# Performance work log

Hardware: AMD Instinct MI355X
Metric: run time of the kernel (lower is better)

The kernel has to match this reference:

```python
import jax, jax.numpy as jnp
import numpy as np

T, B, DIN, DLAT = 512, 128, 256, 512

def setup_inputs() -> dict:
    key = jax.random.key(0)
    k1, k2, k3, k4, k5 = jax.random.split(key, 5)
    s_i = 1.0 / np.sqrt(DIN)
    s_h = 1.0 / np.sqrt(DLAT)
    return {
        "X": jax.random.normal(k1, (T, B, DIN), dtype=jnp.float32),
        "h": jnp.zeros((B, DLAT), dtype=jnp.float32),
        "Wi": jax.random.uniform(k2, (DLAT, DIN), jnp.float32, -s_i, s_i),
        "bi": jax.random.uniform(k3, (DLAT,), jnp.float32, -s_i, s_i),
        "Wh": jax.random.uniform(k4, (DLAT, DLAT), jnp.float32, -s_h, s_h),
        "bh": jax.random.uniform(k5, (DLAT,), jnp.float32, -s_h, s_h),
    }

def reference(X, h, Wi, bi, Wh, bh):
    # Precompute input projection for all timesteps at once: [T,B,DLAT]
    Xi = jnp.einsum('tbd,ld->tbl', X, Wi) + bi + bh
    def step(h_prev, xi_t):
        h_t = jnp.tanh(xi_t + h_prev @ Wh.T)  # [B, DLAT]
        return h_t, h_t
    _, H = jax.lax.scan(step, h, Xi)
    return H  # [T, B, DLAT]
```

## Files before the change

kernel.cpp:

```cpp
#include <hip/hip_runtime.h>

#define T_STEPS 512
#define BATCH   128
#define DIN     256
#define DLAT    512

typedef __bf16 bf16x8 __attribute__((ext_vector_type(8)));
typedef float  f32x4  __attribute__((ext_vector_type(4)));
typedef int    i32x4  __attribute__((ext_vector_type(4)));
typedef unsigned long long u64;

__device__ __forceinline__ unsigned int f2bf2(float a, float b) {
  unsigned int ua = __float_as_uint(a);
  unsigned int ub = __float_as_uint(b);
  ua = (ua + 0x7FFFu + ((ua >> 16) & 1u)) >> 16;
  ub = (ub + 0x7FFFu + ((ub >> 16) & 1u)) >> 16;
  return ua | (ub << 16);
}

__device__ __forceinline__ uint4 pack8(float4 f0, float4 f1) {
  uint4 r;
  r.x = f2bf2(f0.x, f0.y);
  r.y = f2bf2(f0.z, f0.w);
  r.z = f2bf2(f1.x, f1.y);
  r.w = f2bf2(f1.z, f1.w);
  return r;
}

extern "C" __global__ __launch_bounds__(256) void pk_wh(
    const float* __restrict__ Wh, unsigned int* __restrict__ out) {
  int idx = blockIdx.x * 256 + threadIdx.x;
  const float* src = Wh + (long)idx * 8;
  float4 f0 = *(const float4*)src;
  float4 f1 = *(const float4*)(src + 4);
  uint4 v = pack8(f0, f1);
  *(uint4*)(out + (long)idx * 4) = v;
}

extern "C" __global__ __launch_bounds__(256) void xi_gemm(
    const float* __restrict__ X, const float* __restrict__ Wi,
    const float* __restrict__ bi, const float* __restrict__ bh,
    float* __restrict__ XiOut) {
  extern __shared__ char smem[];
  char*  sX    = smem;
  char*  sW    = smem + 65536;
  float* sBias = (float*)(smem + 131072);

  const int tid = threadIdx.x;
  const long m0 = (long)blockIdx.x * 128;
  const int  n0 = blockIdx.y * 128;

  #pragma unroll
  for (int c = 0; c < 16; ++c) {
    int id = c * 256 + tid;
    int r  = id >> 5;
    int kc = (id & 31) << 3;
    const float* sx = X + (m0 + r) * DIN + kc;
    float4 a0 = *(const float4*)sx;
    float4 a1 = *(const float4*)(sx + 4);
    int ax = ((r << 9) + (kc << 1)) ^ ((r & 7) << 4);
    *(uint4*)(sX + ax) = pack8(a0, a1);
    const float* sw = Wi + (n0 + r) * DIN + kc;
    float4 b0 = *(const float4*)sw;
    float4 b1 = *(const float4*)(sw + 4);
    *(uint4*)(sW + ax) = pack8(b0, b1);
  }
  if (tid < 128) sBias[tid] = bi[n0 + tid] + bh[n0 + tid];
  __syncthreads();

  const int w = tid >> 6, lane = tid & 63;
  const int wm = (w >> 1) * 64, wn = (w & 1) * 64;
  const int lm = lane & 15, lq = lane >> 4;

  f32x4 acc[4][4];
  #pragma unroll
  for (int nt = 0; nt < 4; ++nt) {
    float bv = sBias[wn + nt * 16 + lm];
    #pragma unroll
    for (int mt = 0; mt < 4; ++mt) acc[mt][nt] = f32x4{bv, bv, bv, bv};
  }

  #pragma unroll
  for (int k0 = 0; k0 < 8; ++k0) {
    int kb = (k0 << 6) + (lq << 4);
    bf16x8 af[4], bfr[4];
    #pragma unroll
    for (int mt = 0; mt < 4; ++mt) {
      int row = wm + mt * 16 + lm;
      int ax = ((row << 9) + kb) ^ ((row & 7) << 4);
      af[mt] = __builtin_bit_cast(bf16x8, *(uint4*)(sX + ax));
    }
    #pragma unroll
    for (int nt = 0; nt < 4; ++nt) {
      int row = wn + nt * 16 + lm;
      int ax = ((row << 9) + kb) ^ ((row & 7) << 4);
      bfr[nt] = __builtin_bit_cast(bf16x8, *(uint4*)(sW + ax));
    }
    #pragma unroll
    for (int mt = 0; mt < 4; ++mt)
      #pragma unroll
      for (int nt = 0; nt < 4; ++nt)
        acc[mt][nt] = __builtin_amdgcn_mfma_f32_16x16x32_bf16(af[mt], bfr[nt], acc[mt][nt], 0, 0, 0);
  }

  #pragma unroll
  for (int mt = 0; mt < 4; ++mt) {
    #pragma unroll
    for (int e = 0; e < 4; ++e) {
      long m = m0 + wm + mt * 16 + (lq << 2) + e;
      float* dst = XiOut + m * DLAT + n0 + wn + lm;
      #pragma unroll
      for (int nt = 0; nt < 4; ++nt)
        dst[nt * 16] = acc[mt][nt][e];
    }
  }
}

extern "C" __global__ __launch_bounds__(512, 2) void rnn_scan(
    const float* __restrict__ h0, const unsigned short* __restrict__ WhP,
    float* __restrict__ HO, u64* __restrict__ hx,
    unsigned int* __restrict__ flags) {
  __shared__ uint4 sH4[1024];
  char* sH = (char*)sH4;

  const int tid = threadIdx.x;
  const int w = tid >> 6, lane = tid & 63;
  const int lm = lane & 15, lq = lane >> 4;
  const int g  = blockIdx.x & 7;
  const int q  = blockIdx.x >> 3;
  const int r0 = g << 4;
  const int nt = (q << 7) + (w << 4);

  i32x4 wreg[16];
  {
    const unsigned short* base = WhP + (nt + lm) * DLAT + (lq << 3);
    #pragma unroll
    for (int kq = 0; kq < 16; ++kq)
      wreg[kq] = *(const i32x4*)(base + kq * 32);
    #pragma unroll
    for (int kq = 0; kq < 16; ++kq)
      asm("" : "+v"(wreg[kq]));
  }

  #pragma unroll
  for (int c = 0; c < 2; ++c) {
    int id = c * 512 + tid;
    int m = id >> 6, kc = (id & 63) << 3;
    const float* src = h0 + (r0 + m) * DLAT + kc;
    float4 f0 = *(const float4*)src;
    float4 f1 = *(const float4*)(src + 4);
    int ax = ((m << 10) + (kc << 1)) ^ ((m & 7) << 4);
    *(uint4*)(sH + ax) = pack8(f0, f1);
  }
  __syncthreads();

  const int mask  = (lm & 7) << 4;
  const int hbase = (lm << 10) + (lq << 4);
  const int ncol  = nt + (lq << 2);
  unsigned int* flg = flags + (g << 9);

  float4 xi = *(const float4*)(HO + (long)(r0 + lm) * DLAT + ncol);

  for (int t = 0; t < T_STEPS; ++t) {
    f32x4 acc0 = f32x4{0.f, 0.f, 0.f, 0.f};
    f32x4 acc1 = f32x4{0.f, 0.f, 0.f, 0.f};
    #pragma unroll
    for (int kq = 0; kq < 16; kq += 2) {
      int ha0 = (hbase + kq * 64) ^ mask;
      int ha1 = (hbase + (kq + 1) * 64) ^ mask;
      bf16x8 hb0 = __builtin_bit_cast(bf16x8, *(uint4*)(sH + ha0));
      bf16x8 hb1 = __builtin_bit_cast(bf16x8, *(uint4*)(sH + ha1));
      acc0 = __builtin_amdgcn_mfma_f32_16x16x32_bf16(
          __builtin_bit_cast(bf16x8, wreg[kq]), hb0, acc0, 0, 0, 0);
      acc1 = __builtin_amdgcn_mfma_f32_16x16x32_bf16(
          __builtin_bit_cast(bf16x8, wreg[kq + 1]), hb1, acc1, 0, 0, 0);
    }

    float hv[4];
    #pragma unroll
    for (int e = 0; e < 4; ++e) {
      float z = acc0[e] + acc1[e] + ((float*)&xi)[e];
      float ex = __expf(2.0f * z);
      hv[e] = 1.0f - 2.0f / (ex + 1.0f);
    }

    if (t + 1 < T_STEPS) {
      u64* hxg = hx + ((long)(t & 1) << 14) + ((long)g << 11);
      u64 v = ((u64)f2bf2(hv[2], hv[3]) << 32) | (u64)f2bf2(hv[0], hv[1]);

      __hip_atomic_store(&hxg[(lm << 7) + (ncol >> 2)], v,
                         __ATOMIC_RELAXED, __HIP_MEMORY_SCOPE_AGENT);
      asm volatile("s_waitcnt vmcnt(0)" ::: "memory");
      __syncthreads();

      {
        int ax = ((lm << 10) + (ncol << 1)) ^ mask;
        *(u64*)(sH + ax) = v;
      }
      if (tid == 0) {
        __hip_atomic_fetch_add(&flg[t], 1u, __ATOMIC_RELAXED, __HIP_MEMORY_SCOPE_AGENT);
        while (__hip_atomic_load(&flg[t], __ATOMIC_RELAXED, __HIP_MEMORY_SCOPE_AGENT) < 4u)
          __builtin_amdgcn_s_sleep(1);
      }
      __syncthreads();
      asm volatile("" ::: "memory");

      {
        int m = tid >> 5, j = tid & 31;
        #pragma unroll
        for (int s = 1; s < 4; ++s) {
          int qq = (q + s) & 3;
          int idx = (m << 7) + (qq << 5) + j;
          u64 hvv = __hip_atomic_load(&hxg[idx],
                                      __ATOMIC_RELAXED, __HIP_MEMORY_SCOPE_AGENT);
          int ax = ((m << 10) + (((qq << 5) + j) << 3)) ^ ((m & 7) << 4);
          *(u64*)(sH + ax) = hvv;
        }
      }

      {
        float4 o; o.x = hv[0]; o.y = hv[1]; o.z = hv[2]; o.w = hv[3];
        *(float4*)(HO + ((long)t * BATCH + r0 + lm) * DLAT + ncol) = o;
        xi = *(const float4*)(HO + ((long)(t + 1) * BATCH + r0 + lm) * DLAT + ncol);
      }

      __syncthreads();
    } else {
      float4 o; o.x = hv[0]; o.y = hv[1]; o.z = hv[2]; o.w = hv[3];
      *(float4*)(HO + ((long)t * BATCH + r0 + lm) * DLAT + ncol) = o;
    }
  }
}

extern "C" void kernel_launch(void* const* d_in, const int* in_sizes, int n_in,
                              void* d_out, int out_size, void* d_ws, size_t ws_size,
                              hipStream_t stream) {
  const float* X  = (const float*)d_in[0];
  const float* h0 = (const float*)d_in[1];
  const float* Wi = (const float*)d_in[2];
  const float* bi = (const float*)d_in[3];
  const float* Wh = (const float*)d_in[4];
  const float* bh = (const float*)d_in[5];
  float* out = (float*)d_out;

  unsigned int* whp   = (unsigned int*)d_ws;
  u64*          hx    = (u64*)((char*)d_ws + 524288);
  unsigned int* flags = (unsigned int*)((char*)d_ws + 786432);

  hipMemsetAsync(flags, 0, 16384, stream);

  hipFuncSetAttribute((const void*)xi_gemm, hipFuncAttributeMaxDynamicSharedMemorySize, 131584);

  pk_wh<<<128, 256, 0, stream>>>(Wh, whp);
  xi_gemm<<<dim3(512, 4), 256, 131584, stream>>>(X, Wi, bi, bh, out);
  rnn_scan<<<32, 512, 0, stream>>>(h0, (const unsigned short*)whp, out, hx, flags);
}
```

Measured before the change: 1.370 ms.

## Replace atomic counter barrier with per-block flags and wave-local polling

The inter-block step barrier changes from a single atomic fetch-add counter polled by thread 0 into one flag per producer block. Every wave polls the three peer flags itself, which removes one __syncthreads per step. The HO store and next-step xi load move ahead of the wait so they overlap it, and the MFMA reduction is split into four independent accumulators for more ILP. This adds more polling traffic and a larger flag buffer to clear. Memory ordering still relies on relaxed atomics plus the existing vmcnt wait.

```diff
diff --git a/kernel.cpp b/kernel.cpp
--- a/kernel.cpp
+++ b/kernel.cpp
@@ -157,29 +157,36 @@
   const int mask  = (lm & 7) << 4;
   const int hbase = (lm << 10) + (lq << 4);
   const int ncol  = nt + (lq << 2);
-  unsigned int* flg = flags + (g << 9);
+  unsigned int* fgrp = flags + (g << 11);
+  const int sq = (q + 1 + lane) & 3;
 
   float4 xi = *(const float4*)(HO + (long)(r0 + lm) * DLAT + ncol);
 
   for (int t = 0; t < T_STEPS; ++t) {
-    f32x4 acc0 = f32x4{0.f, 0.f, 0.f, 0.f};
-    f32x4 acc1 = f32x4{0.f, 0.f, 0.f, 0.f};
-    #pragma unroll
-    for (int kq = 0; kq < 16; kq += 2) {
-      int ha0 = (hbase + kq * 64) ^ mask;
-      int ha1 = (hbase + (kq + 1) * 64) ^ mask;
-      bf16x8 hb0 = __builtin_bit_cast(bf16x8, *(uint4*)(sH + ha0));
-      bf16x8 hb1 = __builtin_bit_cast(bf16x8, *(uint4*)(sH + ha1));
-      acc0 = __builtin_amdgcn_mfma_f32_16x16x32_bf16(
-          __builtin_bit_cast(bf16x8, wreg[kq]), hb0, acc0, 0, 0, 0);
-      acc1 = __builtin_amdgcn_mfma_f32_16x16x32_bf16(
-          __builtin_bit_cast(bf16x8, wreg[kq + 1]), hb1, acc1, 0, 0, 0);
+    f32x4 a0 = f32x4{0.f, 0.f, 0.f, 0.f};
+    f32x4 a1 = f32x4{0.f, 0.f, 0.f, 0.f};
+    f32x4 a2 = f32x4{0.f, 0.f, 0.f, 0.f};
+    f32x4 a3 = f32x4{0.f, 0.f, 0.f, 0.f};
+    #pragma unroll
+    for (int kq = 0; kq < 16; kq += 4) {
+      bf16x8 hb0 = __builtin_bit_cast(bf16x8, *(uint4*)(sH + ((hbase + kq * 64) ^ mask)));
+      bf16x8 hb1 = __builtin_bit_cast(bf16x8, *(uint4*)(sH + ((hbase + (kq + 1) * 64) ^ mask)));
+      bf16x8 hb2 = __builtin_bit_cast(bf16x8, *(uint4*)(sH + ((hbase + (kq + 2) * 64) ^ mask)));
+      bf16x8 hb3 = __builtin_bit_cast(bf16x8, *(uint4*)(sH + ((hbase + (kq + 3) * 64) ^ mask)));
+      a0 = __builtin_amdgcn_mfma_f32_16x16x32_bf16(
+          __builtin_bit_cast(bf16x8, wreg[kq]), hb0, a0, 0, 0, 0);
+      a1 = __builtin_amdgcn_mfma_f32_16x16x32_bf16(
+          __builtin_bit_cast(bf16x8, wreg[kq + 1]), hb1, a1, 0, 0, 0);
+      a2 = __builtin_amdgcn_mfma_f32_16x16x32_bf16(
+          __builtin_bit_cast(bf16x8, wreg[kq + 2]), hb2, a2, 0, 0, 0);
+      a3 = __builtin_amdgcn_mfma_f32_16x16x32_bf16(
+          __builtin_bit_cast(bf16x8, wreg[kq + 3]), hb3, a3, 0, 0, 0);
     }
 
     float hv[4];
     #pragma unroll
     for (int e = 0; e < 4; ++e) {
-      float z = acc0[e] + acc1[e] + ((float*)&xi)[e];
+      float z = (a0[e] + a1[e]) + (a2[e] + a3[e]) + ((float*)&xi)[e];
       float ex = __expf(2.0f * z);
       hv[e] = 1.0f - 2.0f / (ex + 1.0f);
     }
@@ -193,16 +200,25 @@
       asm volatile("s_waitcnt vmcnt(0)" ::: "memory");
       __syncthreads();
 
+      if (tid == 0)
+        __hip_atomic_store(&fgrp[(q << 9) + t], 1u,
+                           __ATOMIC_RELAXED, __HIP_MEMORY_SCOPE_AGENT);
+
       {
         int ax = ((lm << 10) + (ncol << 1)) ^ mask;
         *(u64*)(sH + ax) = v;
+        float4 o; o.x = hv[0]; o.y = hv[1]; o.z = hv[2]; o.w = hv[3];
+        *(float4*)(HO + ((long)t * BATCH + r0 + lm) * DLAT + ncol) = o;
+        xi = *(const float4*)(HO + ((long)(t + 1) * BATCH + r0 + lm) * DLAT + ncol);
       }
-      if (tid == 0) {
-        __hip_atomic_fetch_add(&flg[t], 1u, __ATOMIC_RELAXED, __HIP_MEMORY_SCOPE_AGENT);
-        while (__hip_atomic_load(&flg[t], __ATOMIC_RELAXED, __HIP_MEMORY_SCOPE_AGENT) < 4u)
-          __builtin_amdgcn_s_sleep(1);
+
+      for (;;) {
+        unsigned int fv = (lane < 3)
+            ? __hip_atomic_load(&fgrp[(sq << 9) + t], __ATOMIC_RELAXED, __HIP_MEMORY_SCOPE_AGENT)
+            : 1u;
+        if (!__any(fv == 0u)) break;
+        __builtin_amdgcn_s_sleep(1);
       }
-      __syncthreads();
       asm volatile("" ::: "memory");
 
       {
@@ -218,12 +234,6 @@
         }
       }
 
-      {
-        float4 o; o.x = hv[0]; o.y = hv[1]; o.z = hv[2]; o.w = hv[3];
-        *(float4*)(HO + ((long)t * BATCH + r0 + lm) * DLAT + ncol) = o;
-        xi = *(const float4*)(HO + ((long)(t + 1) * BATCH + r0 + lm) * DLAT + ncol);
-      }
-
       __syncthreads();
     } else {
       float4 o; o.x = hv[0]; o.y = hv[1]; o.z = hv[2]; o.w = hv[3];
@@ -247,7 +257,7 @@
   u64*          hx    = (u64*)((char*)d_ws + 524288);
   unsigned int* flags = (unsigned int*)((char*)d_ws + 786432);
 
-  hipMemsetAsync(flags, 0, 16384, stream);
+  hipMemsetAsync(flags, 0, 65536, stream);
 
   hipFuncSetAttribute((const void*)xi_gemm, hipFuncAttributeMaxDynamicSharedMemorySize, 131584);
 
```

Result: faster. 1.306 ms (-4.7%).
